# Performance work log

Measured on AMD Instinct MI355X. Metric: run time of the kernel, lower is better.

Reference implementation:

```python
import jax, jax.numpy as jnp
import numpy as np

CAPE_DIM, ERA5_DIM, ATTN_DIM = 128, 256, 128
B, H, W = 8, 64, 64


def setup_inputs() -> dict:
    key = jax.random.key(0)
    ks = jax.random.split(key, 12)
    s = 0.02
    return {
        "cape_features": jax.random.normal(ks[0], (B, CAPE_DIM, H, W), jnp.float32),
        "era5_features": jax.random.normal(ks[1], (B, ERA5_DIM, H, W), jnp.float32),
        "Wq": jax.random.normal(ks[2], (ATTN_DIM, CAPE_DIM), jnp.float32) * s,
        "bq": jax.random.normal(ks[3], (ATTN_DIM,), jnp.float32) * s,
        "Wk": jax.random.normal(ks[4], (ATTN_DIM, ERA5_DIM), jnp.float32) * s,
        "bk": jax.random.normal(ks[5], (ATTN_DIM,), jnp.float32) * s,
        "Wv": jax.random.normal(ks[6], (ATTN_DIM, ERA5_DIM), jnp.float32) * s,
        "bv": jax.random.normal(ks[7], (ATTN_DIM,), jnp.float32) * s,
        "Wo": jax.random.normal(ks[8], (CAPE_DIM, ATTN_DIM), jnp.float32) * s,
        "bo": jax.random.normal(ks[9], (CAPE_DIM,), jnp.float32) * s,
    }


def reference(cape_features, era5_features, Wq, bq, Wk, bk, Wv, bv, Wo, bo):
    b, c, h, w = cape_features.shape
    n = h * w
    cape = cape_features.reshape(b, c, n)          # [B, Cc, N]
    era5 = era5_features.reshape(b, era5_features.shape[1], n)  # [B, Ce, N]
    # 1x1 convs == channel-wise linear projections
    q = jnp.einsum('oc,bcn->bon', Wq, cape) + bq[None, :, None]  # [B, D, N]
    k = jnp.einsum('oc,bcn->bon', Wk, era5) + bk[None, :, None]  # [B, D, N]
    v = jnp.einsum('oc,bcn->bon', Wv, era5) + bv[None, :, None]  # [B, D, N]
    scale = Wq.shape[0] ** (-0.5)
    attn = jnp.einsum('bdq,bdk->bqk', q, k) * scale              # [B, Nq, Nk]
    attn = jax.nn.softmax(attn, axis=-1)
    out = jnp.einsum('bdk,bqk->bdq', v, attn)                    # [B, D, Nq]
    out = jnp.einsum('od,bdn->bon', Wo, out) + bo[None, :, None]  # [B, Cc, N]
    return out.reshape(b, c, h, w)
```

## Files before the change

kernel.cpp:

```cpp
#include <hip/hip_runtime.h>

typedef unsigned short u16;
typedef __attribute__((ext_vector_type(8))) short short8;
typedef __attribute__((ext_vector_type(4))) float f32x4;
typedef __attribute__((ext_vector_type(16))) float f32x16;

constexpr int BATCH = 8, CC = 128, CE = 256, DIM = 128, NTOK = 4096;
constexpr int KSPLIT = 2, KVB = 64, KTILES = NTOK / KSPLIT / KVB;
constexpr float KSC = 0.088388347648318447f * 1.4426950408889634f;

#define DEV static __device__ __forceinline__

DEV u16 f2bf(float f) {
    union { float f; unsigned u; } v; v.f = f;
    unsigned r = (v.u + 0x7fffu + ((v.u >> 16) & 1u)) >> 16;
    return (u16)r;
}
DEV float bf2f(u16 h) {
    union { unsigned u; float f; } v; v.u = ((unsigned)h) << 16;
    return v.f;
}
DEV short8 mk8(unsigned a, unsigned b, unsigned c, unsigned d) {
    union { unsigned u[4]; short8 s; } t; t.u[0] = a; t.u[1] = b; t.u[2] = c; t.u[3] = d;
    return t.s;
}

__global__ __launch_bounds__(256)
void xpose_kernel(const float* __restrict__ cape, const float* __restrict__ era5,
                  u16* __restrict__ capeT, u16* __restrict__ era5T)
{
    __shared__ __align__(16) u16 sT[64 * 68];
    const int tid = threadIdx.x;
    const int nbase = blockIdx.x * 64;
    const int ct = blockIdx.y;
    const int b = blockIdx.z;

    const float* src; u16* dst; int pitch, c0;
    if (ct < 2) { src = cape + ((size_t)b * CC + ct * 64) * NTOK;
                  dst = capeT + (size_t)b * NTOK * CC; pitch = CC; c0 = ct * 64; }
    else        { src = era5 + ((size_t)b * CE + (ct - 2) * 64) * NTOK;
                  dst = era5T + (size_t)b * NTOK * CE; pitch = CE; c0 = (ct - 2) * 64; }

#pragma unroll
    for (int i = 0; i < 4; ++i) {
        int lin = tid + 256 * i;
        int c = lin >> 4, n4 = (lin & 15) * 4;
        float4 v = *(const float4*)&src[(size_t)c * NTOK + nbase + n4];
        ushort4 h; h.x = f2bf(v.x); h.y = f2bf(v.y); h.z = f2bf(v.z); h.w = f2bf(v.w);
        *(ushort4*)&sT[c * 68 + n4] = h;
    }
    __syncthreads();
#pragma unroll
    for (int i = 0; i < 2; ++i) {
        int lin = tid + 256 * i;
        int n = lin >> 3, cs = (lin & 7) * 8;
        short8 o;
#pragma unroll
        for (int j = 0; j < 8; ++j) o[j] = (short)sT[(cs + j) * 68 + n];
        *(short8*)&dst[(size_t)(nbase + n) * pitch + c0 + cs] = o;
    }
}

__global__ __launch_bounds__(256)
void wconv_kernel(const float* __restrict__ Wq, const float* __restrict__ Wk,
                  const float* __restrict__ Wv, const float* __restrict__ Wo,
                  u16* __restrict__ Wqb, u16* __restrict__ Wkb,
                  u16* __restrict__ Wvb, u16* __restrict__ Wob)
{
    int lin = (blockIdx.x * 256 + threadIdx.x) * 4;
    const float* s; u16* d; int off; float sc;
    if (lin < 16384)      { s = Wq; d = Wqb; off = lin; sc = KSC; }
    else if (lin < 49152) { s = Wk; d = Wkb; off = lin - 16384; sc = 1.f; }
    else if (lin < 81920) { s = Wv; d = Wvb; off = lin - 49152; sc = 1.f; }
    else                  { s = Wo; d = Wob; off = lin - 81920; sc = 1.f; }
    float4 v = *(const float4*)&s[off];
    ushort4 h; h.x = f2bf(v.x * sc); h.y = f2bf(v.y * sc);
    h.z = f2bf(v.z * sc); h.w = f2bf(v.w * sc);
    *(ushort4*)&d[off] = h;
}

__global__ __launch_bounds__(256)
void qkv_proj_kernel(const u16* __restrict__ capeT, const u16* __restrict__ era5T,
                     const u16* __restrict__ Wqb, const u16* __restrict__ Wkb,
                     const u16* __restrict__ Wvb, const float* __restrict__ bq,
                     const float* __restrict__ bk, const float* __restrict__ bv,
                     u16* __restrict__ Qb, u16* __restrict__ Kb, u16* __restrict__ Vb)
{
    __shared__ __align__(16) u16 sT[4][32 * 68];

    const int tid = threadIdx.x, lane = tid & 63, w = tid >> 6;
    const int l31 = lane & 31, half = lane >> 5;
    const int b = blockIdx.y, nbase = blockIdx.x * 64;
    const int d = w * 32 + l31;

    f32x16 aq0, aq1;
#pragma unroll
    for (int r = 0; r < 16; ++r) { aq0[r] = 0.f; aq1[r] = 0.f; }
    {
        const u16* xr0 = capeT + ((size_t)b * NTOK + nbase + l31) * CC + half * 8;
        const u16* xr1 = xr0 + 32 * CC;
        const u16* wr  = Wqb + (size_t)d * CC + half * 8;
#pragma unroll
        for (int kc = 0; kc < 8; ++kc) {
            short8 a0 = *(const short8*)(xr0 + kc * 16);
            short8 a1 = *(const short8*)(xr1 + kc * 16);
            short8 bw = *(const short8*)(wr + kc * 16);
            aq0 = __builtin_amdgcn_mfma_f32_32x32x16_bf16(a0, bw, aq0, 0, 0, 0);
            aq1 = __builtin_amdgcn_mfma_f32_32x32x16_bf16(a1, bw, aq1, 0, 0, 0);
        }
    }
    {
        const float bias = bq[d] * KSC;
        u16* q0 = Qb + ((size_t)b * NTOK + nbase) * DIM + d;
#pragma unroll
        for (int r = 0; r < 16; ++r) {
            const int nl = (r & 3) + 8 * (r >> 2) + 4 * half;
            q0[(size_t)nl * DIM] = f2bf(aq0[r] + bias);
            q0[(size_t)(nl + 32) * DIM] = f2bf(aq1[r] + bias);
        }
    }

    f32x16 ak0, ak1, av0, av1;
#pragma unroll
    for (int r = 0; r < 16; ++r) { ak0[r] = 0.f; ak1[r] = 0.f; av0[r] = 0.f; av1[r] = 0.f; }
    {
        const u16* er0 = era5T + ((size_t)b * NTOK + nbase + l31) * CE + half * 8;
        const u16* er1 = er0 + 32 * CE;
        const u16* wkr = Wkb + (size_t)d * CE + half * 8;
        const u16* wvr = Wvb + (size_t)d * CE + half * 8;
#pragma unroll
        for (int kc = 0; kc < 16; ++kc) {
            short8 a0 = *(const short8*)(er0 + kc * 16);
            short8 a1 = *(const short8*)(er1 + kc * 16);
            short8 bwk = *(const short8*)(wkr + kc * 16);
            short8 bwv = *(const short8*)(wvr + kc * 16);
            ak0 = __builtin_amdgcn_mfma_f32_32x32x16_bf16(a0, bwk, ak0, 0, 0, 0);
            ak1 = __builtin_amdgcn_mfma_f32_32x32x16_bf16(a1, bwk, ak1, 0, 0, 0);
            av0 = __builtin_amdgcn_mfma_f32_32x32x16_bf16(a0, bwv, av0, 0, 0, 0);
            av1 = __builtin_amdgcn_mfma_f32_32x32x16_bf16(a1, bwv, av1, 0, 0, 0);
        }
    }
    {
        const float bias = bk[d];
        u16* k0 = Kb + ((size_t)b * NTOK + nbase) * DIM + d;
#pragma unroll
        for (int r = 0; r < 16; ++r) {
            const int nl = (r & 3) + 8 * (r >> 2) + 4 * half;
            k0[(size_t)nl * DIM] = f2bf(ak0[r] + bias);
            k0[(size_t)(nl + 32) * DIM] = f2bf(ak1[r] + bias);
        }
    }
    {
        const float bias = bv[d];
        u16* t = &sT[w][0];
#pragma unroll
        for (int r = 0; r < 16; ++r) {
            const int nl = (r & 3) + 8 * (r >> 2) + 4 * half;
            t[l31 * 68 + nl] = f2bf(av0[r] + bias);
            t[l31 * 68 + nl + 32] = f2bf(av1[r] + bias);
        }
#pragma unroll
        for (int i = 0; i < 4; ++i) {
            int rlin = lane + 64 * i;
            int dl = rlin >> 3, n8 = (rlin & 7) * 8;
            uint2 p0 = *(const uint2*)&t[dl * 68 + n8];
            uint2 p1 = *(const uint2*)&t[dl * 68 + n8 + 4];
            uint4 o = {p0.x, p0.y, p1.x, p1.y};
            *(uint4*)&Vb[((size_t)b * DIM + w * 32 + dl) * NTOK + nbase + n8] = o;
        }
    }
}

__global__ __launch_bounds__(256, 2)
void attn_kernel(const u16* __restrict__ Qb, const u16* __restrict__ Kb,
                 const u16* __restrict__ Vb, u16* __restrict__ Op,
                 float* __restrict__ Lp)
{
    __shared__ __align__(16) u16 sK[2][KVB * 128];
    __shared__ __align__(16) u16 sV[2][128 * KVB];

    const int tid = threadIdx.x;
    const int lane = tid & 63, w = tid >> 6;
    const int l31 = lane & 31, half = lane >> 5;

    const int lin = blockIdx.x;
    const int b = lin & 7;
    const int r2 = lin >> 3;
    const int ks = r2 & 1;
    const int qt = r2 >> 1;
    const int qbase = qt * 128 + w * 32;
    const int kbase = ks * (NTOK / KSPLIT);

    const u16* Kbat = Kb + (size_t)b * NTOK * DIM;
    const u16* Vbat = Vb + (size_t)b * DIM * NTOK;

#define STAGE(bufK, bufV, tt)                                                          \
    {                                                                                  \
        const u16* kb0 = Kbat + (size_t)(kbase + (tt) * KVB) * DIM;                    \
        _Pragma("unroll")                                                              \
        for (int i = 0; i < 4; ++i) {                                                  \
            const int row = w * 16 + i * 4 + (lane >> 4);                              \
            const int p = lane & 15;                                                   \
            const u16* g = kb0 + (size_t)row * DIM + ((p ^ (row & 7)) * 8);            \
            __builtin_amdgcn_global_load_lds(                                          \
                (const __attribute__((address_space(1))) unsigned int*)g,              \
                (__attribute__((address_space(3))) unsigned int*)&(bufK)[(w * 16 + i * 4) * 128], \
                16, 0, 0);                                                             \
        }                                                                              \
        const u16* vb0 = Vbat + kbase + (tt) * KVB;                                    \
        _Pragma("unroll")                                                              \
        for (int i = 0; i < 4; ++i) {                                                  \
            const int row = w * 32 + i * 8 + (lane >> 3);                              \
            const int p = lane & 7;                                                    \
            const u16* g = vb0 + (size_t)row * NTOK + ((p ^ (row & 7)) * 8);           \
            __builtin_amdgcn_global_load_lds(                                          \
                (const __attribute__((address_space(1))) unsigned int*)g,              \
                (__attribute__((address_space(3))) unsigned int*)&(bufV)[(w * 32 + i * 8) * 64], \
                16, 0, 0);                                                             \
        }                                                                              \
    }

    short8 aQ[8];
    {
        const u16* qrow = Qb + ((size_t)b * NTOK + qbase + l31) * DIM + half * 8;
#pragma unroll
        for (int s = 0; s < 8; ++s) aQ[s] = *(const short8*)&qrow[s * 16];
    }

    STAGE(sK[0], sV[0], 0);
    STAGE(sK[1], sV[1], 1);

    f32x16 O[4];
#pragma unroll
    for (int i = 0; i < 4; ++i)
#pragma unroll
        for (int r = 0; r < 16; ++r) O[i][r] = 0.f;
    f32x16 SA0, SA1, SB0, SB1;
#pragma unroll
    for (int r = 0; r < 16; ++r) { SA0[r] = 0.f; SA1[r] = 0.f; }
    float lA = 0.f;

    asm volatile("s_waitcnt vmcnt(8)" ::: "memory");
    __builtin_amdgcn_s_barrier();
    __builtin_amdgcn_sched_barrier(0);
    __builtin_amdgcn_s_setprio(1);
#pragma unroll
    for (int s = 0; s < 8; ++s) {
        const int pos = (((s * 2 + half) ^ (l31 & 7)) * 8);
        short8 k0 = *(const short8*)&sK[0][l31 * 128 + pos];
        short8 k1 = *(const short8*)&sK[0][(32 + l31) * 128 + pos];
        SA0 = __builtin_amdgcn_mfma_f32_32x32x16_bf16(k0, aQ[s], SA0, 0, 0, 0);
        SA1 = __builtin_amdgcn_mfma_f32_32x32x16_bf16(k1, aQ[s], SA1, 0, 0, 0);
    }
    __builtin_amdgcn_s_setprio(0);

#define SM_ONE(s, SC0, SC1)                                                           \
    {                                                                                 \
        float p0 = __builtin_amdgcn_exp2f(((s) < 4 ? (SC0) : (SC1))[((s) & 3) * 4 + 0]); \
        float p1 = __builtin_amdgcn_exp2f(((s) < 4 ? (SC0) : (SC1))[((s) & 3) * 4 + 1]); \
        float p2 = __builtin_amdgcn_exp2f(((s) < 4 ? (SC0) : (SC1))[((s) & 3) * 4 + 2]); \
        float p3 = __builtin_amdgcn_exp2f(((s) < 4 ? (SC0) : (SC1))[((s) & 3) * 4 + 3]); \
        lA += (p0 + p1) + (p2 + p3);                                                  \
        asm("v_cvt_pk_bf16_f32 %0, %1, %2" : "=v"(xm[s]) : "v"(p0), "v"(p1));         \
        asm("v_cvt_pk_bf16_f32 %0, %1, %2" : "=v"(ym[s]) : "v"(p2), "v"(p3));         \
    }

#define BODY(t, SC0, SC1, SN0, SN1)                                                   \
    {                                                                                 \
        const bool hasNext = ((t) + 1 < KTILES);                                      \
        if (hasNext) {                                                                \
            asm volatile("s_waitcnt vmcnt(0)" ::: "memory");                          \
            __builtin_amdgcn_s_barrier();                                             \
            __builtin_amdgcn_sched_barrier(0);                                        \
        }                                                                             \
        const u16* sKn = &sK[((t) + 1) & 1][0];                                       \
        const u16* sVc = &sV[(t) & 1][0];                                             \
        unsigned xm[8], ym[8];                                                        \
        if (hasNext) {                                                                \
            _Pragma("unroll")                                                         \
            for (int r = 0; r < 16; ++r) { (SN0)[r] = 0.f; (SN1)[r] = 0.f; }          \
            __builtin_amdgcn_s_setprio(1);                                            \
            _Pragma("unroll")                                                         \
            for (int s = 0; s < 8; ++s) {                                             \
                const int pos = (((s * 2 + half) ^ (l31 & 7)) * 8);                   \
                short8 k0 = *(const short8*)&sKn[l31 * 128 + pos];                    \
                short8 k1 = *(const short8*)&sKn[(32 + l31) * 128 + pos];             \
                (SN0) = __builtin_amdgcn_mfma_f32_32x32x16_bf16(k0, aQ[s], (SN0), 0, 0, 0); \
                (SN1) = __builtin_amdgcn_mfma_f32_32x32x16_bf16(k1, aQ[s], (SN1), 0, 0, 0); \
                SM_ONE(s, SC0, SC1)                                                   \
            }                                                                         \
            __builtin_amdgcn_s_setprio(0);                                            \
        } else {                                                                      \
            _Pragma("unroll")                                                         \
            for (int s = 0; s < 8; ++s) SM_ONE(s, SC0, SC1)                           \
        }                                                                             \
        short8 pa[4];                                                                 \
        _Pragma("unroll")                                                             \
        for (int s2 = 0; s2 < 4; ++s2) {                                              \
            unsigned xa = xm[2 * s2], xb = xm[2 * s2 + 1];                            \
            unsigned ya = ym[2 * s2], yb = ym[2 * s2 + 1];                            \
            asm("v_permlane32_swap_b32 %0, %1" : "+v"(xa), "+v"(xb));                 \
            asm("v_permlane32_swap_b32 %0, %1" : "+v"(ya), "+v"(yb));                 \
            pa[s2] = mk8(xa, ya, xb, yb);                                             \
        }                                                                             \
        __builtin_amdgcn_s_setprio(1);                                                \
        _Pragma("unroll")                                                             \
        for (int dblk = 0; dblk < 4; ++dblk) {                                        \
            const int vrow = dblk * 32 + l31;                                         \
            _Pragma("unroll")                                                         \
            for (int s2 = 0; s2 < 4; ++s2) {                                          \
                short8 v = *(const short8*)&sVc[vrow * 64 + (((s2 * 2 + half) ^ (l31 & 7)) * 8)]; \
                O[dblk] = __builtin_amdgcn_mfma_f32_32x32x16_bf16(pa[s2], v, O[dblk], 0, 0, 0); \
            }                                                                         \
        }                                                                             \
        __builtin_amdgcn_s_setprio(0);                                                \
        __builtin_amdgcn_sched_barrier(0);                                            \
        __builtin_amdgcn_s_barrier();                                                 \
        __builtin_amdgcn_sched_barrier(0);                                            \
        if ((t) + 2 < KTILES) STAGE(sK[(t) & 1], sV[(t) & 1], (t) + 2);               \
    }

#pragma unroll 1
    for (int tp = 0; tp < KTILES; tp += 2) {
        BODY(tp,     SA0, SA1, SB0, SB1)
        BODY(tp + 1, SB0, SB1, SA0, SA1)
    }
#undef BODY
#undef SM_ONE
#undef STAGE

    float lt = lA + __shfl_xor(lA, 32, 64);
    if (half == 0) {
        float* lp = Lp + (size_t)(ks * BATCH + b) * NTOK + qbase;
        lp[l31] = lt;
    }

    u16* obase = Op + ((size_t)(ks * BATCH + b) * NTOK + qbase) * DIM;
#pragma unroll
    for (int dblk = 0; dblk < 4; ++dblk)
#pragma unroll
        for (int r = 0; r < 16; ++r) {
            const int q = (r & 3) + 8 * (r >> 2) + 4 * half;
            obase[(size_t)q * DIM + dblk * 32 + l31] = f2bf(O[dblk][r]);
        }
}

__global__ __launch_bounds__(256)
void oproj_kernel(const u16* __restrict__ Op, const float* __restrict__ Lp,
                  const u16* __restrict__ Wob, const float* __restrict__ bo,
                  float* __restrict__ Out)
{
    __shared__ __align__(16) u16 sA[64 * 128];

    const int tid = threadIdx.x, lane = tid & 63, w = tid >> 6;
    const int l31 = lane & 31, half = lane >> 5;
    const int b = blockIdx.y;
    const int nbase = blockIdx.x * 64;

#pragma unroll
    for (int i = 0; i < 4; ++i) {
        int idx = tid + 256 * i;
        int c = idx & 15, n = idx >> 4;
        const size_t r0 = ((size_t)b * NTOK + nbase + n) * DIM + c * 8;
        const size_t r1 = ((size_t)(BATCH + b) * NTOK + nbase + n) * DIM + c * 8;
        uint4 v0 = *(const uint4*)&Op[r0];
        uint4 v1 = *(const uint4*)&Op[r1];
        float l = Lp[(size_t)b * NTOK + nbase + n] +
                  Lp[(size_t)(BATCH + b) * NTOK + nbase + n];
        float inv = 1.f / l;
        unsigned t0[4] = {v0.x, v0.y, v0.z, v0.w};
        unsigned t1[4] = {v1.x, v1.y, v1.z, v1.w};
        short8 o;
#pragma unroll
        for (int j = 0; j < 8; ++j) {
            float a  = bf2f((u16)(t0[j >> 1] >> ((j & 1) * 16)));
            float a2 = bf2f((u16)(t1[j >> 1] >> ((j & 1) * 16)));
            o[j] = (short)f2bf((a + a2) * inv);
        }
        *(short8*)&sA[n * 128 + ((c ^ (n & 7)) * 8)] = o;
    }
    __syncthreads();

    const int co = w * 32 + l31;
    const u16* wr = Wob + (size_t)co * DIM + half * 8;
    f32x16 acc0, acc1;
#pragma unroll
    for (int r = 0; r < 16; ++r) { acc0[r] = 0.f; acc1[r] = 0.f; }
#pragma unroll
    for (int kc = 0; kc < 8; ++kc) {
        const int ch = kc * 2 + half;
        short8 a0 = *(const short8*)&sA[l31 * 128 + ((ch ^ (l31 & 7)) * 8)];
        short8 a1 = *(const short8*)&sA[(32 + l31) * 128 + ((ch ^ (l31 & 7)) * 8)];
        short8 bw = *(const short8*)(wr + kc * 16);
        acc0 = __builtin_amdgcn_mfma_f32_32x32x16_bf16(a0, bw, acc0, 0, 0, 0);
        acc1 = __builtin_amdgcn_mfma_f32_32x32x16_bf16(a1, bw, acc1, 0, 0, 0);
    }

    const float bb = bo[co];
    float* ob = Out + ((size_t)b * DIM + co) * NTOK + nbase;
#pragma unroll
    for (int r = 0; r < 16; ++r) {
        const int n = (r & 3) + 8 * (r >> 2) + 4 * half;
        ob[n] = acc0[r] + bb;
        ob[n + 32] = acc1[r] + bb;
    }
}

extern "C" void kernel_launch(void* const* d_in, const int* in_sizes, int n_in,
                              void* d_out, int out_size, void* d_ws, size_t ws_size,
                              hipStream_t stream)
{
    const float* cape = (const float*)d_in[0];
    const float* era5 = (const float*)d_in[1];
    const float* Wq = (const float*)d_in[2];
    const float* bq = (const float*)d_in[3];
    const float* Wk = (const float*)d_in[4];
    const float* bk = (const float*)d_in[5];
    const float* Wv = (const float*)d_in[6];
    const float* bv = (const float*)d_in[7];
    const float* Wo = (const float*)d_in[8];
    const float* bo = (const float*)d_in[9];

    const size_t QKV = (size_t)BATCH * NTOK * DIM;
    u16* Qb  = (u16*)d_ws;
    u16* Kb  = Qb + QKV;
    u16* Vb  = Kb + QKV;
    u16* Wqb = Vb + QKV;
    u16* Wkb = Wqb + 16384;
    u16* Wvb = Wkb + 32768;
    u16* Wob = Wvb + 32768;
    u16* regionA = Wob + 16384;
    u16* capeT = regionA;
    u16* era5T = capeT + QKV;
    u16* Op = regionA;
    float* Lp = (float*)(Op + (size_t)KSPLIT * QKV);

    hipLaunchKernelGGL(xpose_kernel, dim3(64, 6, BATCH), dim3(256), 0, stream,
                       cape, era5, capeT, era5T);
    hipLaunchKernelGGL(wconv_kernel, dim3(96), dim3(256), 0, stream,
                       Wq, Wk, Wv, Wo, Wqb, Wkb, Wvb, Wob);
    hipLaunchKernelGGL(qkv_proj_kernel, dim3(64, BATCH), dim3(256), 0, stream,
                       capeT, era5T, Wqb, Wkb, Wvb, bq, bk, bv, Qb, Kb, Vb);
    hipLaunchKernelGGL(attn_kernel, dim3((NTOK / 128) * KSPLIT * BATCH), dim3(256), 0, stream,
                       Qb, Kb, Vb, Op, Lp);
    hipLaunchKernelGGL(oproj_kernel, dim3(64, BATCH), dim3(256), 0, stream,
                       Op, Lp, Wob, bo, (float*)d_out);
}
```

Measured before the change: 120.3 us.

## Split attention keys four ways with 32-token KV tiles and three blocks per CU

Raises the key split from 2 to 4 and halves the KV tile to 32 tokens. This shrinks LDS per block and S accumulators, allowing three resident blocks per CU and twice as many blocks in the grid. Staging loads, the V swizzle, the softmax macros and the output projection's partial-sum reduction are all adapted to the new split. In exchange it writes and reads twice as many bf16 partial outputs and adds per-tile barrier overhead with less MFMA work between syncs.

```diff
diff --git a/kernel.cpp b/kernel.cpp
--- a/kernel.cpp
+++ b/kernel.cpp
@@ -6,7 +6,7 @@
 typedef __attribute__((ext_vector_type(16))) float f32x16;
 
 constexpr int BATCH = 8, CC = 128, CE = 256, DIM = 128, NTOK = 4096;
-constexpr int KSPLIT = 2, KVB = 64, KTILES = NTOK / KSPLIT / KVB;
+constexpr int KSPLIT = 4, KVB = 32, KTILES = NTOK / KSPLIT / KVB;
 constexpr float KSC = 0.088388347648318447f * 1.4426950408889634f;
 
 #define DEV static __device__ __forceinline__
@@ -171,7 +171,7 @@
     }
 }
 
-__global__ __launch_bounds__(256, 2)
+__global__ __launch_bounds__(256, 3)
 void attn_kernel(const u16* __restrict__ Qb, const u16* __restrict__ Kb,
                  const u16* __restrict__ Vb, u16* __restrict__ Op,
                  float* __restrict__ Lp)
@@ -185,9 +185,9 @@
 
     const int lin = blockIdx.x;
     const int b = lin & 7;
-    const int r2 = lin >> 3;
-    const int ks = r2 & 1;
-    const int qt = r2 >> 1;
+    const int rem = lin >> 3;
+    const int qt = rem & 31;
+    const int ks = rem >> 5;
     const int qbase = qt * 128 + w * 32;
     const int kbase = ks * (NTOK / KSPLIT);
 
@@ -198,24 +198,24 @@
     {                                                                                  \
         const u16* kb0 = Kbat + (size_t)(kbase + (tt) * KVB) * DIM;                    \
         _Pragma("unroll")                                                              \
-        for (int i = 0; i < 4; ++i) {                                                  \
-            const int row = w * 16 + i * 4 + (lane >> 4);                              \
+        for (int i = 0; i < 2; ++i) {                                                  \
+            const int row = w * 8 + i * 4 + (lane >> 4);                               \
             const int p = lane & 15;                                                   \
             const u16* g = kb0 + (size_t)row * DIM + ((p ^ (row & 7)) * 8);            \
             __builtin_amdgcn_global_load_lds(                                          \
                 (const __attribute__((address_space(1))) unsigned int*)g,              \
-                (__attribute__((address_space(3))) unsigned int*)&(bufK)[(w * 16 + i * 4) * 128], \
+                (__attribute__((address_space(3))) unsigned int*)&(bufK)[(w * 8 + i * 4) * 128], \
                 16, 0, 0);                                                             \
         }                                                                              \
         const u16* vb0 = Vbat + kbase + (tt) * KVB;                                    \
         _Pragma("unroll")                                                              \
-        for (int i = 0; i < 4; ++i) {                                                  \
-            const int row = w * 32 + i * 8 + (lane >> 3);                              \
-            const int p = lane & 7;                                                    \
-            const u16* g = vb0 + (size_t)row * NTOK + ((p ^ (row & 7)) * 8);           \
+        for (int i = 0; i < 2; ++i) {                                                  \
+            const int row = w * 32 + i * 16 + (lane >> 2);                             \
+            const int p = lane & 3;                                                    \
+            const u16* g = vb0 + (size_t)row * NTOK + ((p ^ (row & 3)) * 8);           \
             __builtin_amdgcn_global_load_lds(                                          \
                 (const __attribute__((address_space(1))) unsigned int*)g,              \
-                (__attribute__((address_space(3))) unsigned int*)&(bufV)[(w * 32 + i * 8) * 64], \
+                (__attribute__((address_space(3))) unsigned int*)&(bufV)[(w * 32 + i * 16) * KVB], \
                 16, 0, 0);                                                             \
         }                                                                              \
     }
@@ -235,12 +235,12 @@
     for (int i = 0; i < 4; ++i)
 #pragma unroll
         for (int r = 0; r < 16; ++r) O[i][r] = 0.f;
-    f32x16 SA0, SA1, SB0, SB1;
-#pragma unroll
-    for (int r = 0; r < 16; ++r) { SA0[r] = 0.f; SA1[r] = 0.f; }
+    f32x16 SA, SB;
+#pragma unroll
+    for (int r = 0; r < 16; ++r) SA[r] = 0.f;
     float lA = 0.f;
 
-    asm volatile("s_waitcnt vmcnt(8)" ::: "memory");
+    asm volatile("s_waitcnt vmcnt(4)" ::: "memory");
     __builtin_amdgcn_s_barrier();
     __builtin_amdgcn_sched_barrier(0);
     __builtin_amdgcn_s_setprio(1);
@@ -248,24 +248,22 @@
     for (int s = 0; s < 8; ++s) {
         const int pos = (((s * 2 + half) ^ (l31 & 7)) * 8);
         short8 k0 = *(const short8*)&sK[0][l31 * 128 + pos];
-        short8 k1 = *(const short8*)&sK[0][(32 + l31) * 128 + pos];
-        SA0 = __builtin_amdgcn_mfma_f32_32x32x16_bf16(k0, aQ[s], SA0, 0, 0, 0);
-        SA1 = __builtin_amdgcn_mfma_f32_32x32x16_bf16(k1, aQ[s], SA1, 0, 0, 0);
+        SA = __builtin_amdgcn_mfma_f32_32x32x16_bf16(k0, aQ[s], SA, 0, 0, 0);
     }
     __builtin_amdgcn_s_setprio(0);
 
-#define SM_ONE(s, SC0, SC1)                                                           \
+#define SM_ONE(s, SC)                                                                 \
     {                                                                                 \
-        float p0 = __builtin_amdgcn_exp2f(((s) < 4 ? (SC0) : (SC1))[((s) & 3) * 4 + 0]); \
-        float p1 = __builtin_amdgcn_exp2f(((s) < 4 ? (SC0) : (SC1))[((s) & 3) * 4 + 1]); \
-        float p2 = __builtin_amdgcn_exp2f(((s) < 4 ? (SC0) : (SC1))[((s) & 3) * 4 + 2]); \
-        float p3 = __builtin_amdgcn_exp2f(((s) < 4 ? (SC0) : (SC1))[((s) & 3) * 4 + 3]); \
+        float p0 = __builtin_amdgcn_exp2f((SC)[(s) * 4 + 0]);                         \
+        float p1 = __builtin_amdgcn_exp2f((SC)[(s) * 4 + 1]);                         \
+        float p2 = __builtin_amdgcn_exp2f((SC)[(s) * 4 + 2]);                         \
+        float p3 = __builtin_amdgcn_exp2f((SC)[(s) * 4 + 3]);                         \
         lA += (p0 + p1) + (p2 + p3);                                                  \
         asm("v_cvt_pk_bf16_f32 %0, %1, %2" : "=v"(xm[s]) : "v"(p0), "v"(p1));         \
         asm("v_cvt_pk_bf16_f32 %0, %1, %2" : "=v"(ym[s]) : "v"(p2), "v"(p3));         \
     }
 
-#define BODY(t, SC0, SC1, SN0, SN1)                                                   \
+#define BODY(t, SC, SN)                                                               \
     {                                                                                 \
         const bool hasNext = ((t) + 1 < KTILES);                                      \
         if (hasNext) {                                                                \
@@ -275,28 +273,26 @@
         }                                                                             \
         const u16* sKn = &sK[((t) + 1) & 1][0];                                       \
         const u16* sVc = &sV[(t) & 1][0];                                             \
-        unsigned xm[8], ym[8];                                                        \
+        unsigned xm[4], ym[4];                                                        \
         if (hasNext) {                                                                \
             _Pragma("unroll")                                                         \
-            for (int r = 0; r < 16; ++r) { (SN0)[r] = 0.f; (SN1)[r] = 0.f; }          \
+            for (int r = 0; r < 16; ++r) (SN)[r] = 0.f;                               \
             __builtin_amdgcn_s_setprio(1);                                            \
             _Pragma("unroll")                                                         \
             for (int s = 0; s < 8; ++s) {                                             \
                 const int pos = (((s * 2 + half) ^ (l31 & 7)) * 8);                   \
                 short8 k0 = *(const short8*)&sKn[l31 * 128 + pos];                    \
-                short8 k1 = *(const short8*)&sKn[(32 + l31) * 128 + pos];             \
-                (SN0) = __builtin_amdgcn_mfma_f32_32x32x16_bf16(k0, aQ[s], (SN0), 0, 0, 0); \
-                (SN1) = __builtin_amdgcn_mfma_f32_32x32x16_bf16(k1, aQ[s], (SN1), 0, 0, 0); \
-                SM_ONE(s, SC0, SC1)                                                   \
+                (SN) = __builtin_amdgcn_mfma_f32_32x32x16_bf16(k0, aQ[s], (SN), 0, 0, 0); \
+                if ((s) < 4) SM_ONE(s, SC)                                            \
             }                                                                         \
             __builtin_amdgcn_s_setprio(0);                                            \
         } else {                                                                      \
             _Pragma("unroll")                                                         \
-            for (int s = 0; s < 8; ++s) SM_ONE(s, SC0, SC1)                           \
+            for (int s = 0; s < 4; ++s) SM_ONE(s, SC)                                 \
         }                                                                             \
-        short8 pa[4];                                                                 \
+        short8 pa[2];                                                                 \
         _Pragma("unroll")                                                             \
-        for (int s2 = 0; s2 < 4; ++s2) {                                              \
+        for (int s2 = 0; s2 < 2; ++s2) {                                              \
             unsigned xa = xm[2 * s2], xb = xm[2 * s2 + 1];                            \
             unsigned ya = ym[2 * s2], yb = ym[2 * s2 + 1];                            \
             asm("v_permlane32_swap_b32 %0, %1" : "+v"(xa), "+v"(xb));                 \
@@ -308,8 +304,8 @@
         for (int dblk = 0; dblk < 4; ++dblk) {                                        \
             const int vrow = dblk * 32 + l31;                                         \
             _Pragma("unroll")                                                         \
-            for (int s2 = 0; s2 < 4; ++s2) {                                          \
-                short8 v = *(const short8*)&sVc[vrow * 64 + (((s2 * 2 + half) ^ (l31 & 7)) * 8)]; \
+            for (int s2 = 0; s2 < 2; ++s2) {                                          \
+                short8 v = *(const short8*)&sVc[vrow * KVB + (((s2 * 2 + half) ^ (vrow & 3)) * 8)]; \
                 O[dblk] = __builtin_amdgcn_mfma_f32_32x32x16_bf16(pa[s2], v, O[dblk], 0, 0, 0); \
             }                                                                         \
         }                                                                             \
@@ -322,8 +318,8 @@
 
 #pragma unroll 1
     for (int tp = 0; tp < KTILES; tp += 2) {
-        BODY(tp,     SA0, SA1, SB0, SB1)
-        BODY(tp + 1, SB0, SB1, SA0, SA1)
+        BODY(tp,     SA, SB)
+        BODY(tp + 1, SB, SA)
     }
 #undef BODY
 #undef SM_ONE
@@ -361,22 +357,24 @@
     for (int i = 0; i < 4; ++i) {
         int idx = tid + 256 * i;
         int c = idx & 15, n = idx >> 4;
-        const size_t r0 = ((size_t)b * NTOK + nbase + n) * DIM + c * 8;
-        const size_t r1 = ((size_t)(BATCH + b) * NTOK + nbase + n) * DIM + c * 8;
-        uint4 v0 = *(const uint4*)&Op[r0];
-        uint4 v1 = *(const uint4*)&Op[r1];
-        float l = Lp[(size_t)b * NTOK + nbase + n] +
-                  Lp[(size_t)(BATCH + b) * NTOK + nbase + n];
+        float acc[8];
+#pragma unroll
+        for (int j = 0; j < 8; ++j) acc[j] = 0.f;
+        float l = 0.f;
+#pragma unroll
+        for (int ks = 0; ks < KSPLIT; ++ks) {
+            const size_t rr = ((size_t)(ks * BATCH + b) * NTOK + nbase + n) * DIM + c * 8;
+            uint4 v = *(const uint4*)&Op[rr];
+            unsigned tt[4] = {v.x, v.y, v.z, v.w};
+#pragma unroll
+            for (int j = 0; j < 8; ++j)
+                acc[j] += bf2f((u16)(tt[j >> 1] >> ((j & 1) * 16)));
+            l += Lp[(size_t)(ks * BATCH + b) * NTOK + nbase + n];
+        }
         float inv = 1.f / l;
-        unsigned t0[4] = {v0.x, v0.y, v0.z, v0.w};
-        unsigned t1[4] = {v1.x, v1.y, v1.z, v1.w};
         short8 o;
 #pragma unroll
-        for (int j = 0; j < 8; ++j) {
-            float a  = bf2f((u16)(t0[j >> 1] >> ((j & 1) * 16)));
-            float a2 = bf2f((u16)(t1[j >> 1] >> ((j & 1) * 16)));
-            o[j] = (short)f2bf((a + a2) * inv);
-        }
+        for (int j = 0; j < 8; ++j) o[j] = (short)f2bf(acc[j] * inv);
         *(short8*)&sA[n * 128 + ((c ^ (n & 7)) * 8)] = o;
     }
     __syncthreads();
```

Result: slower. 171.5 us (+42.6%).

## Fuse input transpose and bf16 conversion into QKV projection kernel

Applied to the files above, without the earlier changes.

Removes the separate transpose kernel that wrote bf16 token-major copies of cape and era5. The projection kernel now reads fp32 channel-major inputs directly, converts each 64-channel chunk to bf16 in shared memory, and gathers the MFMA operands from there. This drops one kernel launch and a full write-then-read round trip of the transposed inputs through global memory. In exchange it adds per-chunk barriers and scalar strided shared-memory gathers, and the grid is only 512 blocks, so load latency is less hidden.

```diff
diff --git a/kernel.cpp b/kernel.cpp
--- a/kernel.cpp
+++ b/kernel.cpp
@@ -23,42 +23,6 @@
 DEV short8 mk8(unsigned a, unsigned b, unsigned c, unsigned d) {
     union { unsigned u[4]; short8 s; } t; t.u[0] = a; t.u[1] = b; t.u[2] = c; t.u[3] = d;
     return t.s;
-}
-
-__global__ __launch_bounds__(256)
-void xpose_kernel(const float* __restrict__ cape, const float* __restrict__ era5,
-                  u16* __restrict__ capeT, u16* __restrict__ era5T)
-{
-    __shared__ __align__(16) u16 sT[64 * 68];
-    const int tid = threadIdx.x;
-    const int nbase = blockIdx.x * 64;
-    const int ct = blockIdx.y;
-    const int b = blockIdx.z;
-
-    const float* src; u16* dst; int pitch, c0;
-    if (ct < 2) { src = cape + ((size_t)b * CC + ct * 64) * NTOK;
-                  dst = capeT + (size_t)b * NTOK * CC; pitch = CC; c0 = ct * 64; }
-    else        { src = era5 + ((size_t)b * CE + (ct - 2) * 64) * NTOK;
-                  dst = era5T + (size_t)b * NTOK * CE; pitch = CE; c0 = (ct - 2) * 64; }
-
-#pragma unroll
-    for (int i = 0; i < 4; ++i) {
-        int lin = tid + 256 * i;
-        int c = lin >> 4, n4 = (lin & 15) * 4;
-        float4 v = *(const float4*)&src[(size_t)c * NTOK + nbase + n4];
-        ushort4 h; h.x = f2bf(v.x); h.y = f2bf(v.y); h.z = f2bf(v.z); h.w = f2bf(v.w);
-        *(ushort4*)&sT[c * 68 + n4] = h;
-    }
-    __syncthreads();
-#pragma unroll
-    for (int i = 0; i < 2; ++i) {
-        int lin = tid + 256 * i;
-        int n = lin >> 3, cs = (lin & 7) * 8;
-        short8 o;
-#pragma unroll
-        for (int j = 0; j < 8; ++j) o[j] = (short)sT[(cs + j) * 68 + n];
-        *(short8*)&dst[(size_t)(nbase + n) * pitch + c0 + cs] = o;
-    }
 }
 
 __global__ __launch_bounds__(256)
@@ -80,12 +44,13 @@
 }
 
 __global__ __launch_bounds__(256)
-void qkv_proj_kernel(const u16* __restrict__ capeT, const u16* __restrict__ era5T,
-                     const u16* __restrict__ Wqb, const u16* __restrict__ Wkb,
-                     const u16* __restrict__ Wvb, const float* __restrict__ bq,
-                     const float* __restrict__ bk, const float* __restrict__ bv,
-                     u16* __restrict__ Qb, u16* __restrict__ Kb, u16* __restrict__ Vb)
+void qkv_fused_kernel(const float* __restrict__ cape, const float* __restrict__ era5,
+                      const u16* __restrict__ Wqb, const u16* __restrict__ Wkb,
+                      const u16* __restrict__ Wvb, const float* __restrict__ bq,
+                      const float* __restrict__ bk, const float* __restrict__ bv,
+                      u16* __restrict__ Qb, u16* __restrict__ Kb, u16* __restrict__ Vb)
 {
+    __shared__ __align__(16) u16 sX[64 * 68];
     __shared__ __align__(16) u16 sT[4][32 * 68];
 
     const int tid = threadIdx.x, lane = tid & 63, w = tid >> 6;
@@ -93,20 +58,46 @@
     const int b = blockIdx.y, nbase = blockIdx.x * 64;
     const int d = w * 32 + l31;
 
+#define STAGE_X(srcbase)                                                      \
+    {                                                                         \
+        _Pragma("unroll")                                                     \
+        for (int i = 0; i < 4; ++i) {                                         \
+            int lin = tid + 256 * i;                                          \
+            int c = lin >> 4, n4 = (lin & 15) * 4;                            \
+            float4 v = *(const float4*)&(srcbase)[(size_t)c * NTOK + n4];     \
+            ushort4 h; h.x = f2bf(v.x); h.y = f2bf(v.y);                      \
+            h.z = f2bf(v.z); h.w = f2bf(v.w);                                 \
+            *(ushort4*)&sX[c * 68 + n4] = h;                                  \
+        }                                                                     \
+    }
+#define GATHER(kcl, a0, a1)                                                   \
+    {                                                                         \
+        _Pragma("unroll")                                                     \
+        for (int j = 0; j < 8; ++j) {                                         \
+            int c = (kcl) * 16 + half * 8 + j;                                \
+            (a0)[j] = (short)sX[c * 68 + l31];                                \
+            (a1)[j] = (short)sX[c * 68 + 32 + l31];                           \
+        }                                                                     \
+    }
+
     f32x16 aq0, aq1;
 #pragma unroll
     for (int r = 0; r < 16; ++r) { aq0[r] = 0.f; aq1[r] = 0.f; }
     {
-        const u16* xr0 = capeT + ((size_t)b * NTOK + nbase + l31) * CC + half * 8;
-        const u16* xr1 = xr0 + 32 * CC;
-        const u16* wr  = Wqb + (size_t)d * CC + half * 8;
-#pragma unroll
-        for (int kc = 0; kc < 8; ++kc) {
-            short8 a0 = *(const short8*)(xr0 + kc * 16);
-            short8 a1 = *(const short8*)(xr1 + kc * 16);
-            short8 bw = *(const short8*)(wr + kc * 16);
-            aq0 = __builtin_amdgcn_mfma_f32_32x32x16_bf16(a0, bw, aq0, 0, 0, 0);
-            aq1 = __builtin_amdgcn_mfma_f32_32x32x16_bf16(a1, bw, aq1, 0, 0, 0);
+        const u16* wq = Wqb + (size_t)d * CC + half * 8;
+#pragma unroll 1
+        for (int q = 0; q < 2; ++q) {
+            if (q) __syncthreads();
+            STAGE_X(cape + ((size_t)b * CC + q * 64) * NTOK + nbase);
+            __syncthreads();
+#pragma unroll
+            for (int kcl = 0; kcl < 4; ++kcl) {
+                short8 a0, a1;
+                GATHER(kcl, a0, a1);
+                short8 bw = *(const short8*)(wq + (q * 4 + kcl) * 16);
+                aq0 = __builtin_amdgcn_mfma_f32_32x32x16_bf16(a0, bw, aq0, 0, 0, 0);
+                aq1 = __builtin_amdgcn_mfma_f32_32x32x16_bf16(a1, bw, aq1, 0, 0, 0);
+            }
         }
     }
     {
@@ -124,20 +115,24 @@
 #pragma unroll
     for (int r = 0; r < 16; ++r) { ak0[r] = 0.f; ak1[r] = 0.f; av0[r] = 0.f; av1[r] = 0.f; }
     {
-        const u16* er0 = era5T + ((size_t)b * NTOK + nbase + l31) * CE + half * 8;
-        const u16* er1 = er0 + 32 * CE;
-        const u16* wkr = Wkb + (size_t)d * CE + half * 8;
-        const u16* wvr = Wvb + (size_t)d * CE + half * 8;
-#pragma unroll
-        for (int kc = 0; kc < 16; ++kc) {
-            short8 a0 = *(const short8*)(er0 + kc * 16);
-            short8 a1 = *(const short8*)(er1 + kc * 16);
-            short8 bwk = *(const short8*)(wkr + kc * 16);
-            short8 bwv = *(const short8*)(wvr + kc * 16);
-            ak0 = __builtin_amdgcn_mfma_f32_32x32x16_bf16(a0, bwk, ak0, 0, 0, 0);
-            ak1 = __builtin_amdgcn_mfma_f32_32x32x16_bf16(a1, bwk, ak1, 0, 0, 0);
-            av0 = __builtin_amdgcn_mfma_f32_32x32x16_bf16(a0, bwv, av0, 0, 0, 0);
-            av1 = __builtin_amdgcn_mfma_f32_32x32x16_bf16(a1, bwv, av1, 0, 0, 0);
+        const u16* wk = Wkb + (size_t)d * CE + half * 8;
+        const u16* wv = Wvb + (size_t)d * CE + half * 8;
+#pragma unroll 1
+        for (int e = 0; e < 4; ++e) {
+            __syncthreads();
+            STAGE_X(era5 + ((size_t)b * CE + e * 64) * NTOK + nbase);
+            __syncthreads();
+#pragma unroll
+            for (int kcl = 0; kcl < 4; ++kcl) {
+                short8 a0, a1;
+                GATHER(kcl, a0, a1);
+                short8 bwk = *(const short8*)(wk + (e * 4 + kcl) * 16);
+                short8 bwv = *(const short8*)(wv + (e * 4 + kcl) * 16);
+                ak0 = __builtin_amdgcn_mfma_f32_32x32x16_bf16(a0, bwk, ak0, 0, 0, 0);
+                ak1 = __builtin_amdgcn_mfma_f32_32x32x16_bf16(a1, bwk, ak1, 0, 0, 0);
+                av0 = __builtin_amdgcn_mfma_f32_32x32x16_bf16(a0, bwv, av0, 0, 0, 0);
+                av1 = __builtin_amdgcn_mfma_f32_32x32x16_bf16(a1, bwv, av1, 0, 0, 0);
+            }
         }
     }
     {
@@ -169,6 +164,8 @@
             *(uint4*)&Vb[((size_t)b * DIM + w * 32 + dl) * NTOK + nbase + n8] = o;
         }
     }
+#undef STAGE_X
+#undef GATHER
 }
 
 __global__ __launch_bounds__(256, 2)
@@ -429,18 +426,13 @@
     u16* Wkb = Wqb + 16384;
     u16* Wvb = Wkb + 32768;
     u16* Wob = Wvb + 32768;
-    u16* regionA = Wob + 16384;
-    u16* capeT = regionA;
-    u16* era5T = capeT + QKV;
-    u16* Op = regionA;
+    u16* Op  = Wob + 16384;
     float* Lp = (float*)(Op + (size_t)KSPLIT * QKV);
 
-    hipLaunchKernelGGL(xpose_kernel, dim3(64, 6, BATCH), dim3(256), 0, stream,
-                       cape, era5, capeT, era5T);
     hipLaunchKernelGGL(wconv_kernel, dim3(96), dim3(256), 0, stream,
                        Wq, Wk, Wv, Wo, Wqb, Wkb, Wvb, Wob);
-    hipLaunchKernelGGL(qkv_proj_kernel, dim3(64, BATCH), dim3(256), 0, stream,
-                       capeT, era5T, Wqb, Wkb, Wvb, bq, bk, bv, Qb, Kb, Vb);
+    hipLaunchKernelGGL(qkv_fused_kernel, dim3(64, BATCH), dim3(256), 0, stream,
+                       cape, era5, Wqb, Wkb, Wvb, bq, bk, bv, Qb, Kb, Vb);
     hipLaunchKernelGGL(attn_kernel, dim3((NTOK / 128) * KSPLIT * BATCH), dim3(256), 0, stream,
                        Qb, Kb, Vb, Op, Lp);
     hipLaunchKernelGGL(oproj_kernel, dim3(64, BATCH), dim3(256), 0, stream,
```

Measured after the change: 108.4 us. -9.9%, faster.
